# Kernel tuning notes

Measured on AMD Instinct MI355X. Metric: run time of the kernel, lower is better.

The kernel has to match this reference:

```python
import jax, jax.numpy as jnp
import numpy as np

SIZE = 128
WIN = SIZE // 4   # sliding-window size == region size (32)
HALF = WIN // 2   # 16


def _conv(x, w, pad, groups=1):
    return jax.lax.conv_general_dilated(x, w, (1, 1), [(pad, pad), (pad, pad)],
        dimension_numbers=('NCHW', 'OIHW', 'NCHW'), feature_group_count=groups)


def _resize(x, h, w):
    # F.interpolate(..., mode='bilinear', align_corners=False)
    return jax.image.resize(x, (x.shape[0], x.shape[1], h, w), 'bilinear', antialias=False)


def _gauss_kernels():
    ax = np.linspace(-2.0, 2.0, 5)
    xx, yy = np.meshgrid(ax, ax)
    g = np.exp(-(xx ** 2 + yy ** 2) / 2.0) / (2.0 * np.pi)  # sigma = 1
    gx = (-xx * g).astype(np.float32)
    gy = (-yy * g).astype(np.float32)
    return (jnp.asarray(np.tile(gx[None, None], (3, 3, 1, 1))),
            jnp.asarray(np.tile(gy[None, None], (3, 3, 1, 1))))


def _edge_extract(x):
    Gx, Gy = _gauss_kernels()
    h = _conv(x, Gx, 2)
    v = _conv(x, Gy, 2)
    return jnp.tanh(jnp.sqrt(h * h + v * v + 1e-8))


def _color_moments(x, win=5):
    # F.unfold-based local mean / unbiased var / skewness, via depthwise box sums
    C = x.shape[1]
    n = float(win * win)
    ones = jnp.ones((C, 1, win, win), x.dtype)
    box = lambda z: _conv(z, ones, win // 2, groups=C)
    s1 = box(x); s2 = box(x * x); s3 = box(x * x * x)
    mean = s1 / n
    var = (s2 - n * mean * mean) / (n - 1.0)               # unbiased, matches torch.var
    m3 = (s3 - 3.0 * mean * s2 + 2.0 * n * mean ** 3) / n  # E[(x-m)^3]
    skew = m3 / (jnp.sqrt(jnp.maximum(var, 0.0)) ** 3 + 1e-6)
    return jnp.concatenate([mean, var, skew], 1)


def _locate_region(c):
    # scipy: gradient magnitude < 0.2 -> 4-connected label at argmax -> bbox center
    H, W = c.shape
    flat = jnp.argmax(c)
    xm = (flat // W).astype(jnp.int32)
    ym = (flat % W).astype(jnp.int32)
    gm = jnp.hypot(jnp.gradient(c, axis=0), jnp.gradient(c, axis=1))
    mask = gm < 0.2
    seed = jnp.zeros((H, W), bool).at[xm, ym].set(True) & mask

    def dil(r):
        d = r
        d = d | jnp.pad(r[1:, :], ((0, 1), (0, 0)))
        d = d | jnp.pad(r[:-1, :], ((1, 0), (0, 0)))
        d = d | jnp.pad(r[:, 1:], ((0, 0), (0, 1)))
        d = d | jnp.pad(r[:, :-1], ((0, 0), (1, 0)))
        return d & mask

    def body(s):
        r, _ = s
        nr = dil(r)
        return (nr, jnp.any(nr != r))

    region, _ = jax.lax.while_loop(lambda s: s[1], body, (seed, jnp.any(seed)))
    rows = jnp.any(region, 1); cols = jnp.any(region, 0)
    rs = jnp.argmax(rows); re = H - jnp.argmax(rows[::-1])
    cs = jnp.argmax(cols); ce = W - jnp.argmax(cols[::-1])
    ok = mask[xm, ym]  # label_at_max != 0
    x1 = jnp.where(ok, ((rs + re) // 2).astype(jnp.int32), xm)
    y1 = jnp.where(ok, ((cs + ce) // 2).astype(jnp.int32), ym)
    return x1, y1


def _affine_grid(move, H, W):
    # theta = [[1,0,tx],[0,1,ty]] with (tx,ty)=move, align_corners=False
    bx = (2.0 * jnp.arange(W, dtype=jnp.float32) + 1.0) / W - 1.0
    by = (2.0 * jnp.arange(H, dtype=jnp.float32) + 1.0) / H - 1.0
    gx = bx[None, None, :] + move[:, 0, None, None]
    gy = by[None, :, None] + move[:, 1, None, None]
    return jnp.stack(jnp.broadcast_arrays(gx, gy), -1)  # [B,H,W,2]


def _grid_sample(x, grid):
    # bilinear, zeros padding, align_corners=False (torch defaults)
    B, C, H, W = x.shape
    ix = ((grid[..., 0] + 1.0) * W - 1.0) / 2.0
    iy = ((grid[..., 1] + 1.0) * H - 1.0) / 2.0
    ix0 = jnp.floor(ix).astype(jnp.int32)
    iy0 = jnp.floor(iy).astype(jnp.int32)
    wx1 = ix - ix0; wy1 = iy - iy0
    b = jnp.arange(B)[:, None, None]

    def g(yy, xx):
        valid = ((xx >= 0) & (xx < W) & (yy >= 0) & (yy < H)).astype(x.dtype)
        v = x[b, :, jnp.clip(yy, 0, H - 1), jnp.clip(xx, 0, W - 1)]  # [B,Hg,Wg,C]
        return v * valid[..., None]

    out = (g(iy0, ix0) * ((1 - wy1) * (1 - wx1))[..., None]
         + g(iy0, ix0 + 1) * ((1 - wy1) * wx1)[..., None]
         + g(iy0 + 1, ix0) * (wy1 * (1 - wx1))[..., None]
         + g(iy0 + 1, ix0 + 1) * (wy1 * wx1)[..., None])
    return jnp.transpose(out, (0, 3, 1, 2))


def _bn_relu6(x, w, b):
    # BatchNorm2d in training mode (batch stats, biased var, eps=1e-5) + ReLU6
    m = x.mean((0, 2, 3), keepdims=True)
    v = ((x - m) ** 2).mean((0, 2, 3), keepdims=True)
    y = (x - m) / jnp.sqrt(v + 1e-5) * w[None, :, None, None] + b[None, :, None, None]
    return jnp.clip(y, 0.0, 6.0)


def setup_inputs():
    key = jax.random.key(0)
    ks = jax.random.split(key, 8)
    B, C = 8, 64
    return dict(
        warm_flag=1,
        feat1=jax.random.normal(ks[0], (B, C, SIZE, SIZE), jnp.float32),
        feat2=jax.random.normal(ks[1], (B, C, SIZE, SIZE), jnp.float32),
        cam1=jax.random.uniform(ks[2], (B, 64, 64), jnp.float32),
        cam2=jax.random.uniform(ks[3], (B, 64, 64), jnp.float32),
        f_g=jax.random.uniform(ks[4], (B, 3, 512, 512), jnp.float32),
        f_e=jax.random.uniform(ks[5], (B, 3, 512, 512), jnp.float32),
        conv1_w=jax.random.normal(ks[6], (C, 3, 3, 3), jnp.float32) * 0.1,
        conv1_b=jnp.zeros((C,), jnp.float32),
        conv2_w=jax.random.normal(ks[7], (C, 9, 3, 3), jnp.float32) * 0.1,
        conv2_b=jnp.zeros((C,), jnp.float32),
        bn_w=jnp.ones((C,), jnp.float32),
        bn_b=jnp.zeros((C,), jnp.float32),
    )


def reference(warm_flag, feat1, feat2, cam1, cam2, f_g, f_e,
              conv1_w, conv1_b, conv2_w, conv2_b, bn_w, bn_b):
    B = cam1.shape[0]
    c1 = _resize(cam1[:, None], SIZE, SIZE)
    c2 = _resize(cam2[:, None], SIZE, SIZE)

    if warm_flag == 1:
        # numpy/scipy path in torch is detached from autograd
        c1s = jax.lax.stop_gradient(c1)
        c2s = jax.lax.stop_gradient(c2)
        x1, y1 = jax.vmap(_locate_region)(c1s[:, 0])
        # valid-mode box convolution of cam2 with ones((H//4, W//4)), argmax
        box = jax.lax.conv_general_dilated(c2s, jnp.ones((1, 1, WIN, WIN), c2.dtype), (1, 1),
            'VALID', dimension_numbers=('NCHW', 'OIHW', 'NCHW'))[:, 0]
        Wv = box.shape[-1]
        flat = jnp.argmax(box.reshape(B, -1), -1)
        x2 = (flat // Wv + HALF).astype(jnp.int32)
        y2 = (flat % Wv + HALF).astype(jnp.int32)

        idx = jnp.arange(SIZE)
        def rect(xc, yc):
            r = (idx[None, :] >= jnp.maximum(xc - HALF, 0)[:, None]) & \
                (idx[None, :] < jnp.minimum(xc + HALF, SIZE)[:, None])
            cc = (idx[None, :] >= jnp.maximum(yc - HALF, 0)[:, None]) & \
                 (idx[None, :] < jnp.minimum(yc + HALF, SIZE)[:, None])
            return r[:, None, :, None] & cc[:, None, None, :]
        mask1 = rect(x1, y1).astype(feat1.dtype)
        mask2 = rect(x2, y2).astype(feat2.dtype)
        mi1 = jnp.stack([x1, y1], -1).astype(jnp.float32)
        mi2 = jnp.stack([x2, y2], -1).astype(jnp.float32)
    else:
        mask1 = jnp.zeros_like(feat1)
        mask2 = jnp.zeros_like(feat2)
        mi1 = jnp.zeros((B, 2), jnp.float32)
        mi2 = jnp.zeros((B, 2), jnp.float32)

    cam2_move = (mi2 - mi1) / (SIZE // 2)
    cam1_move = (mi1 - mi2) / (SIZE // 2)
    grid1 = _affine_grid(cam1_move, SIZE, SIZE)
    grid2 = _affine_grid(cam2_move, SIZE, SIZE)

    moments = _resize(_color_moments(f_e), SIZE, SIZE)   # [B,9,128,128]
    edge = _resize(_edge_extract(f_g), SIZE, SIZE)       # [B,3,128,128]
    feat1_edge = jnp.clip(_conv(edge, conv1_w, 1) + conv1_b[None, :, None, None], 0.0, 6.0)
    feat2_color = _conv(moments, conv2_w, 1) + conv2_b[None, :, None, None]

    feat2_move = _grid_sample(feat2_color * mask2, grid2)
    feat1_edge_move = _grid_sample(feat1_edge * mask1, grid1)

    Bc, C, H, W = feat1.shape
    f1 = feat1.reshape(Bc, C, -1)
    f2 = feat2.reshape(Bc, C, -1)
    f2m = feat2_move.reshape(Bc, C, -1)
    f1m = feat1_edge_move.reshape(Bc, C, -1)

    f2_attn = jax.nn.softmax(jnp.einsum('bcn,bdn->bcd', f2m, f1), -1)  # [B,C,C]
    feat1_apply = jnp.einsum('bcd,bdn->bcn', f2_attn, f1).reshape(Bc, C, H, W)
    f1_attn = jax.nn.softmax(jnp.einsum('bcn,bdn->bcd', f1m, f2), -1)
    feat2_apply = jnp.einsum('bcd,bdn->bcn', f1_attn, f2).reshape(Bc, C, H, W)

    feat1_apply = _bn_relu6(feat1_apply, bn_w, bn_b)
    feat2_apply = _bn_relu6(feat2_apply, bn_w, bn_b)

    if warm_flag == 0:
        return (feat1, feat2, grid1, grid2, feat1_edge, feat2_color, f1_attn, f2_attn, feat1, feat2)
    return (feat1_apply, feat2_apply, grid1, grid2, feat1_edge, feat2_color, f1_attn, f2_attn, feat1, feat2)
```

## Files before the change

kernel.cpp:

```cpp
#include <hip/hip_runtime.h>
#include <math.h>

#define SIZE 128
#define WIN 32
#define HALF 16
#define B 8
#define C 64
#define N (SIZE*SIZE)
#define BCN 8388608
#define BV 97

#define O_APPLY1   0
#define O_APPLY2   8388608
#define O_GRID1    16777216
#define O_GRID2    17039360
#define O_EDGEF    17301504
#define O_COLORF   25690112
#define O_ATTN1    34078720
#define O_ATTN2    34111488
#define O_FEAT1    34144256
#define O_FEAT2    42532864

#define WS_BNP     0
#define WS_XY      361472
#define WS_MOM     361600
#define WS_EDGE    1541248
#define WS_BN      1737856

#define NEGINF (-3.402823466e+38f)

typedef unsigned __int128 u128;

__device__ __forceinline__ u128 hfill(u128 g, u128 m) {
  u128 p = m;
  g |= p & (g << 1);  p &= p << 1;
  g |= p & (g << 2);  p &= p << 2;
  g |= p & (g << 4);  p &= p << 4;
  g |= p & (g << 8);  p &= p << 8;
  g |= p & (g << 16); p &= p << 16;
  g |= p & (g << 32); p &= p << 32;
  g |= p & (g << 64);
  p = m;
  g |= p & (g >> 1);  p &= p >> 1;
  g |= p & (g >> 2);  p &= p >> 2;
  g |= p & (g >> 4);  p &= p >> 4;
  g |= p & (g >> 8);  p &= p >> 8;
  g |= p & (g >> 16); p &= p >> 16;
  g |= p & (g >> 32); p &= p >> 32;
  g |= p & (g >> 64);
  return g;
}

__global__ __launch_bounds__(256) void k_front(
    const float* __restrict__ cam1, const float* __restrict__ cam2,
    int* __restrict__ xy, float* __restrict__ g1, float* __restrict__ g2) {
  int b = blockIdx.x, tid = threadIdx.x;
  __shared__ float sc[N];
  __shared__ float sc2[N];
  __shared__ float sv[256]; __shared__ int si[256];
  __shared__ unsigned int maskw[512];
  __shared__ unsigned long long glo[128], ghi[128];
  __shared__ unsigned long long rowany[2];
  __shared__ int s_changed, s_xm, s_ym, s_ok;
  __shared__ int s_x1, s_y1, s_x2, s_y2;

  const float* src1 = cam1 + b * 4096;
  const float* src2 = cam2 + b * 4096;

  float bv = NEGINF; int bi = 0;
  for (int k = 0; k < 64; ++k) {
    int pix = k * 256 + tid;
    int i = pix >> 7, j = pix & 127;
    float fy = fminf(fmaxf(0.5f * (float)i - 0.25f, 0.f), 63.f);
    float fx = fminf(fmaxf(0.5f * (float)j - 0.25f, 0.f), 63.f);
    int y0 = (int)fy; float ty = fy - (float)y0; int y1i = min(y0 + 1, 63);
    int x0 = (int)fx; float tx = fx - (float)x0; int x1i = min(x0 + 1, 63);
    float a00 = src1[y0 * 64 + x0],  a01 = src1[y0 * 64 + x1i];
    float a10 = src1[y1i * 64 + x0], a11 = src1[y1i * 64 + x1i];
    float v1 = (1.f - ty) * ((1.f - tx) * a00 + tx * a01)
             + ty * ((1.f - tx) * a10 + tx * a11);
    float c00 = src2[y0 * 64 + x0],  c01 = src2[y0 * 64 + x1i];
    float c10 = src2[y1i * 64 + x0], c11 = src2[y1i * 64 + x1i];
    float v2 = (1.f - ty) * ((1.f - tx) * c00 + tx * c01)
             + ty * ((1.f - tx) * c10 + tx * c11);
    sc[pix] = v1; sc2[pix] = v2;
    if (v1 > bv) { bv = v1; bi = pix; }
  }
  sv[tid] = bv; si[tid] = bi;
  __syncthreads();
  for (int s = 128; s; s >>= 1) {
    if (tid < s) {
      float ov = sv[tid + s]; int oi = si[tid + s];
      if (ov > sv[tid] || (ov == sv[tid] && oi < si[tid])) { sv[tid] = ov; si[tid] = oi; }
    }
    __syncthreads();
  }
  if (tid == 0) { s_xm = si[0] >> 7; s_ym = si[0] & 127; }

  #pragma unroll
  for (int q = 0; q < 2; ++q) {
    int w = tid + q * 256;
    int row = w >> 2, cb = (w & 3) * 32;
    unsigned int m = 0;
    for (int bit = 0; bit < 32; ++bit) {
      int i = row, j = cb + bit;
      float gx_, gy_;
      if (i == 0)        gx_ = sc[128 + j] - sc[j];
      else if (i == 127) gx_ = sc[127 * 128 + j] - sc[126 * 128 + j];
      else               gx_ = 0.5f * (sc[(i + 1) * 128 + j] - sc[(i - 1) * 128 + j]);
      if (j == 0)        gy_ = sc[i * 128 + 1] - sc[i * 128];
      else if (j == 127) gy_ = sc[i * 128 + 127] - sc[i * 128 + 126];
      else               gy_ = 0.5f * (sc[i * 128 + j + 1] - sc[i * 128 + j - 1]);
      if (hypotf(gx_, gy_) < 0.2f) m |= (1u << bit);
    }
    maskw[w] = m;
  }
  __syncthreads();
  if (tid == 0) {
    int w = (s_xm << 2) + (s_ym >> 5), bit = s_ym & 31;
    s_ok = (maskw[w] >> bit) & 1;
  }
  __syncthreads();

  int r = tid;
  u128 m = 0, g = 0;
  if (tid < 128) {
    m = ((u128)maskw[r * 4])
      | ((u128)maskw[r * 4 + 1] << 32)
      | ((u128)maskw[r * 4 + 2] << 64)
      | ((u128)maskw[r * 4 + 3] << 96);
    if (s_ok && r == s_xm) g = ((u128)1) << s_ym;
    g = hfill(g, m);
  }
  for (;;) {
    if (tid == 0) s_changed = 0;
    if (tid < 128) { glo[r] = (unsigned long long)g; ghi[r] = (unsigned long long)(g >> 64); }
    __syncthreads();
    if (tid < 128) {
      u128 gn = g;
      if (r > 0)   gn |= ((u128)glo[r - 1]) | ((u128)ghi[r - 1] << 64);
      if (r < 127) gn |= ((u128)glo[r + 1]) | ((u128)ghi[r + 1] << 64);
      gn &= m;
      gn = hfill(gn, m);
      if (gn != g) { g = gn; s_changed = 1; }
    }
    __syncthreads();
    if (!s_changed) break;
  }

  if (tid < 128) {
    unsigned long long ba = __ballot(g != 0);
    if ((tid & 63) == 0) rowany[tid >> 6] = ba;
    glo[r] = (unsigned long long)g; ghi[r] = (unsigned long long)(g >> 64);
  }
  __syncthreads();
  if (tid == 0) {
    unsigned long long r0 = rowany[0], r1 = rowany[1];
    unsigned long long cl = 0, ch = 0;
    for (int i = 0; i < 128; ++i) { cl |= glo[i]; ch |= ghi[i]; }
    int rs = 0, re = 0, cs = 0, ce = 0;
    if (r0 | r1) {
      rs = r0 ? (__ffsll(r0) - 1) : 64 + (__ffsll(r1) - 1);
      re = r1 ? 128 - __clzll(r1) : 64 - __clzll(r0);
      cs = cl ? (__ffsll(cl) - 1) : 64 + (__ffsll(ch) - 1);
      ce = ch ? 128 - __clzll(ch) : 64 - __clzll(cl);
    }
    int x1, y1;
    if (s_ok) { x1 = (rs + re) >> 1; y1 = (cs + ce) >> 1; }
    else      { x1 = s_xm;           y1 = s_ym; }
    xy[b] = x1; xy[8 + b] = y1; s_x1 = x1; s_y1 = y1;
  }
  __syncthreads();

  for (int idx = tid; idx < BV * 128; idx += 256) {
    int rr = idx >> 7, cc = idx & 127;
    float acc = 0.f;
    #pragma unroll
    for (int dy = 0; dy < WIN; ++dy) acc += sc2[(rr + dy) * 128 + cc];
    sc[idx] = acc;
  }
  __syncthreads();

  bv = NEGINF; bi = 0;
  for (int p = tid; p < BV * BV; p += 256) {
    int rr = p / BV, cc = p % BV;
    float s = 0.f;
    #pragma unroll
    for (int dx = 0; dx < WIN; ++dx) s += sc[rr * 128 + cc + dx];
    if (s > bv) { bv = s; bi = p; }
  }
  sv[tid] = bv; si[tid] = bi;
  __syncthreads();
  for (int s = 128; s; s >>= 1) {
    if (tid < s) {
      float ov = sv[tid + s]; int oi = si[tid + s];
      if (ov > sv[tid] || (ov == sv[tid] && oi < si[tid])) { sv[tid] = ov; si[tid] = oi; }
    }
    __syncthreads();
  }
  if (tid == 0) {
    int x2 = si[0] / BV + HALF, y2 = si[0] % BV + HALF;
    xy[16 + b] = x2; xy[24 + b] = y2; s_x2 = x2; s_y2 = y2;
  }
  __syncthreads();

  float x1f = (float)s_x1, y1f = (float)s_y1;
  float x2f = (float)s_x2, y2f = (float)s_y2;
  float m1x = (x1f - x2f) / 64.f, m1y = (y1f - y2f) / 64.f;
  float* g1b = g1 + (size_t)b * N * 2;
  float* g2b = g2 + (size_t)b * N * 2;
  for (int k = 0; k < 64; ++k) {
    int pix = k * 256 + tid;
    int h = pix >> 7, w = pix & 127;
    float bx = (2.f * (float)w + 1.f) / 128.f - 1.f;
    float by = (2.f * (float)h + 1.f) / 128.f - 1.f;
    g1b[pix * 2]     = bx + m1x; g1b[pix * 2 + 1] = by + m1y;
    g2b[pix * 2]     = bx - m1x; g2b[pix * 2 + 1] = by - m1y;
  }
}

__global__ __launch_bounds__(256) void k_prep(const float* __restrict__ fe,
                                              const float* __restrict__ fg,
                                              float* __restrict__ mom,
                                              float* __restrict__ edge) {
  __shared__ float sx[66 * 66];
  int tid = threadIdx.x;
  if (blockIdx.x < 1536) {
    int blk = blockIdx.x;
    int tile = blk & 63, ch = (blk >> 6) % 3, b = blk / 192;
    int ti0 = (tile >> 3) * 16, tj0 = (tile & 7) * 16;
    const float* src = fe + (size_t)(b * 3 + ch) * 262144;
    int oy0 = 4 * ti0 - 1, ox0 = 4 * tj0 - 1;
    for (int l = tid; l < 66 * 66; l += 256) {
      int r = l / 66, cc = l % 66;
      int gy = oy0 + r, gx = ox0 + cc;
      sx[l] = (gy >= 0 && gy < 512 && gx >= 0 && gx < 512) ? src[gy * 512 + gx] : 0.f;
    }
    __syncthreads();
    int ii = tid >> 4, jj = tid & 15;
    int i = ti0 + ii, j = tj0 + jj;
    float s1a[6], s2a[6], s3a[6], s1b[6], s2b[6], s3b[6];
    #pragma unroll
    for (int t = 0; t < 6; ++t) {
      float a1 = 0, a2 = 0, a3 = 0, b1 = 0, b2 = 0, b3 = 0;
      int lx = 4 * jj + t;
      #pragma unroll
      for (int r = 0; r < 6; ++r) {
        float v = sx[(4 * ii + r) * 66 + lx];
        float v2 = v * v, v3 = v2 * v;
        if (r < 5) { a1 += v; a2 += v2; a3 += v3; }
        if (r > 0) { b1 += v; b2 += v2; b3 += v3; }
      }
      s1a[t] = a1; s2a[t] = a2; s3a[t] = a3;
      s1b[t] = b1; s2b[t] = b2; s3b[t] = b3;
    }
    float am = 0, av = 0, as = 0;
    #pragma unroll
    for (int py = 0; py < 2; ++py) {
      #pragma unroll
      for (int px = 0; px < 2; ++px) {
        float s1 = 0, s2 = 0, s3 = 0;
        #pragma unroll
        for (int t = 0; t < 5; ++t) {
          s1 += py ? s1b[px + t] : s1a[px + t];
          s2 += py ? s2b[px + t] : s2a[px + t];
          s3 += py ? s3b[px + t] : s3a[px + t];
        }
        float mean = s1 / 25.f;
        float var  = (s2 - 25.f * mean * mean) / 24.f;
        float m3   = (s3 - 3.f * mean * s2 + 50.f * mean * mean * mean) / 25.f;
        float sq   = sqrtf(fmaxf(var, 0.f));
        float skew = m3 / (sq * sq * sq + 1e-6f);
        am += mean; av += var; as += skew;
      }
    }
    int base = (b * 9 + ch) * N + i * 128 + j;
    mom[base]         = 0.25f * am;
    mom[base + 3 * N] = 0.25f * av;
    mom[base + 6 * N] = 0.25f * as;
  } else {
    int blk = blockIdx.x - 1536;
    int tile = blk & 63, b = blk >> 6;
    int ti0 = (tile >> 3) * 16, tj0 = (tile & 7) * 16;
    const float* s0 = fg + (size_t)b * 3 * 262144;
    int oy0 = 4 * ti0 - 1, ox0 = 4 * tj0 - 1;
    for (int l = tid; l < 66 * 66; l += 256) {
      int r = l / 66, cc = l % 66;
      int gy = oy0 + r, gx = ox0 + cc;
      float v = 0.f;
      if (gy >= 0 && gy < 512 && gx >= 0 && gx < 512) {
        int o = gy * 512 + gx;
        v = s0[o] + s0[262144 + o] + s0[524288 + o];
      }
      sx[l] = v;
    }
    __syncthreads();
    int ii = tid >> 4, jj = tid & 15;
    int i = ti0 + ii, j = tj0 + jj;
    const float INV2PI = 0.15915494309189535f;
    float wg[5], ug[5];
    #pragma unroll
    for (int t = 0; t < 5; ++t) {
      float a = (float)t - 2.f;
      float e = expf(-0.5f * a * a);
      wg[t] = e; ug[t] = -a * e;
    }
    float rAa[6], rAb[6], rBa[6], rBb[6];
    #pragma unroll
    for (int t = 0; t < 6; ++t) {
      float aa = 0, ab = 0, ba = 0, bb = 0;
      int lx = 4 * jj + t;
      #pragma unroll
      for (int r = 0; r < 6; ++r) {
        float v = sx[(4 * ii + r) * 66 + lx];
        if (r < 5) { aa += v * wg[r]; ba += v * ug[r]; }
        if (r > 0) { ab += v * wg[r - 1]; bb += v * ug[r - 1]; }
      }
      rAa[t] = aa; rAb[t] = ab; rBa[t] = ba; rBb[t] = bb;
    }
    float acc = 0.f;
    #pragma unroll
    for (int py = 0; py < 2; ++py) {
      #pragma unroll
      for (int px = 0; px < 2; ++px) {
        float h = 0, v = 0;
        #pragma unroll
        for (int t = 0; t < 5; ++t) {
          float A  = py ? rAb[px + t] : rAa[px + t];
          float Bw = py ? rBb[px + t] : rBa[px + t];
          h += A * ug[t];
          v += Bw * wg[t];
        }
        h *= INV2PI; v *= INV2PI;
        acc += tanhf(sqrtf(h * h + v * v + 1e-8f));
      }
    }
    edge[b * N + i * 128 + j] = 0.25f * acc;
  }
}

__global__ __launch_bounds__(256) void k_conv12(
    const float* __restrict__ edge, const float* __restrict__ w1,
    const float* __restrict__ b1, float* __restrict__ o4,
    const float* __restrict__ mom, const float* __restrict__ w2,
    const float* __restrict__ b2, float* __restrict__ o5) {
  __shared__ float tin[9 * 324];
  __shared__ float wsm[64 * 84];
  int b = blockIdx.x >> 6, tile = blockIdx.x & 63;
  int ti0 = (tile >> 3) * 16, tj0 = (tile & 7) * 16;
  int tid = threadIdx.x;
  int i = tid >> 4, j = tid & 15;
  if (blockIdx.y == 0) {
    for (int l = tid; l < 324; l += 256) {
      int r = l / 18, cc = l % 18;
      int gi = ti0 + r - 1, gj = tj0 + cc - 1;
      tin[l] = (gi >= 0 && gi < 128 && gj >= 0 && gj < 128) ? edge[b * N + gi * 128 + gj] : 0.f;
    }
    for (int l = tid; l < 64 * 12; l += 256) {
      int o = l / 12, t = l % 12;
      wsm[l] = (t < 9) ? (w1[o * 27 + t] + w1[o * 27 + 9 + t] + w1[o * 27 + 18 + t]) : 0.f;
    }
    __syncthreads();
    float win[12];
    #pragma unroll
    for (int dy = 0; dy < 3; ++dy)
      #pragma unroll
      for (int dx = 0; dx < 3; ++dx)
        win[dy * 3 + dx] = tin[(i + dy) * 18 + (j + dx)];
    win[9] = 0.f; win[10] = 0.f; win[11] = 0.f;
    float* o = o4 + (size_t)b * C * N + (ti0 + i) * 128 + tj0 + j;
    for (int oc = 0; oc < C; ++oc) {
      const float4* wr = (const float4*)(wsm + oc * 12);
      float acc = b1[oc];
      #pragma unroll
      for (int q = 0; q < 3; ++q) {
        float4 w4 = wr[q];
        acc += w4.x * win[4 * q] + w4.y * win[4 * q + 1]
             + w4.z * win[4 * q + 2] + w4.w * win[4 * q + 3];
      }
      o[oc * N] = fminf(fmaxf(acc, 0.f), 6.f);
    }
  } else {
    for (int l = tid; l < 9 * 324; l += 256) {
      int ic = l / 324, rem = l % 324, r = rem / 18, cc = rem % 18;
      int gi = ti0 + r - 1, gj = tj0 + cc - 1;
      tin[l] = (gi >= 0 && gi < 128 && gj >= 0 && gj < 128) ? mom[(b * 9 + ic) * N + gi * 128 + gj] : 0.f;
    }
    for (int l = tid; l < 64 * 84; l += 256) {
      int o = l / 84, t = l % 84;
      wsm[l] = (t < 81) ? w2[o * 81 + t] : 0.f;
    }
    __syncthreads();
    float win[84];
    #pragma unroll
    for (int ic = 0; ic < 9; ++ic)
      #pragma unroll
      for (int dy = 0; dy < 3; ++dy)
        #pragma unroll
        for (int dx = 0; dx < 3; ++dx)
          win[ic * 9 + dy * 3 + dx] = tin[ic * 324 + (i + dy) * 18 + (j + dx)];
    win[81] = 0.f; win[82] = 0.f; win[83] = 0.f;
    float* o = o5 + (size_t)b * C * N + (ti0 + i) * 128 + tj0 + j;
    for (int oc = 0; oc < C; ++oc) {
      const float4* wr = (const float4*)(wsm + oc * 84);
      float acc = b2[oc];
      #pragma unroll
      for (int q = 0; q < 21; ++q) {
        float4 w4 = wr[q];
        acc += w4.x * win[4 * q] + w4.y * win[4 * q + 1]
             + w4.z * win[4 * q + 2] + w4.w * win[4 * q + 3];
      }
      o[oc * N] = acc;
    }
  }
}

__global__ __launch_bounds__(256) void k_logits(const float* __restrict__ aB1,
                                                const float* __restrict__ bB1,
                                                const float* __restrict__ aB2,
                                                const float* __restrict__ bB2,
                                                float* __restrict__ lg,
                                                const int* __restrict__ xy) {
  int mode = blockIdx.y;
  const float* aBase = mode ? aB2 : aB1;
  const float* bBase = mode ? bB2 : bB1;
  int b = blockIdx.x >> 4, sl = blockIdx.x & 15;
  int tid = threadIdx.x;
  int ci = (tid >> 4) << 2, di = (tid & 15) << 2;
  float* o = lg + (size_t)(((mode * 8 + b) * 16 + sl)) * 4096;

  int x1 = xy[b], y1 = xy[8 + b], x2 = xy[16 + b], y2 = xy[24 + b];
  int dyh, dxw, rlo, rhi, clo, chi;
  if (mode == 0) {
    dyh = y1 - y2; dxw = x1 - x2;
    rlo = max(x1 - HALF, 0); rhi = min(x1 + HALF, SIZE);
    clo = max(y1 - HALF, 0); chi = min(y1 + HALF, SIZE);
  } else {
    dyh = y2 - y1; dxw = x2 - x1;
    rlo = max(x2 - HALF, 0); rhi = min(x2 + HALF, SIZE);
    clo = max(y2 - HALF, 0); chi = min(y2 + HALF, SIZE);
  }
  int hlo = max(0, rlo - dyh), hhi = min(SIZE, rhi - dyh);
  int wlo = max(0, clo - dxw), whi = min(SIZE, chi - dxw);
  int wn = whi - wlo, hn = hhi - hlo;
  int npos = (wn > 0 && hn > 0) ? wn * hn : 0;
  if (sl * 64 >= npos) {
    #pragma unroll
    for (int u = 0; u < 4; ++u)
      #pragma unroll
      for (int v = 0; v < 4; ++v)
        o[(ci + u) * 64 + (di + v)] = 0.f;
    return;
  }

  __shared__ float aS[64][65];
  __shared__ float bS[64][65];
  const float* aB = aBase + (size_t)b * C * N;
  const float* bB = bBase + (size_t)b * C * N;
  for (int l = tid; l < 4096; l += 256) {
    int ch = l >> 6, k = l & 63;
    int p = sl * 64 + k;
    float av = 0.f, bv = 0.f;
    if (p < npos) {
      int h = hlo + p / wn, w = wlo + p % wn;
      av = aB[ch * N + (h + dyh) * 128 + (w + dxw)];
      bv = bB[ch * N + h * 128 + w];
    }
    aS[ch][k] = av; bS[ch][k] = bv;
  }
  __syncthreads();
  float acc[4][4] = {};
  #pragma unroll 4
  for (int k = 0; k < 64; ++k) {
    float a0 = aS[ci][k], a1 = aS[ci + 1][k], a2 = aS[ci + 2][k], a3 = aS[ci + 3][k];
    float b0 = bS[di][k], b1v = bS[di + 1][k], b2v = bS[di + 2][k], b3 = bS[di + 3][k];
    acc[0][0] += a0 * b0; acc[0][1] += a0 * b1v; acc[0][2] += a0 * b2v; acc[0][3] += a0 * b3;
    acc[1][0] += a1 * b0; acc[1][1] += a1 * b1v; acc[1][2] += a1 * b2v; acc[1][3] += a1 * b3;
    acc[2][0] += a2 * b0; acc[2][1] += a2 * b1v; acc[2][2] += a2 * b2v; acc[2][3] += a2 * b3;
    acc[3][0] += a3 * b0; acc[3][1] += a3 * b1v; acc[3][2] += a3 * b2v; acc[3][3] += a3 * b3;
  }
  #pragma unroll
  for (int u = 0; u < 4; ++u)
    #pragma unroll
    for (int v = 0; v < 4; ++v)
      o[(ci + u) * 64 + (di + v)] = acc[u][v];
}

__global__ void k_softmax(const float* __restrict__ lg,
                          float* __restrict__ o6, float* __restrict__ o7) {
  int row = blockIdx.x;
  int mode = blockIdx.y;
  float* dst = mode ? o7 : o6;
  int b = row >> 6, c = row & 63;
  int lane = threadIdx.x;
  const float* base = lg + (size_t)((mode * 8 + b) * 16) * 4096 + c * 64 + lane;
  float v = 0.f;
  #pragma unroll
  for (int sl = 0; sl < 16; ++sl) v += base[sl * 4096];
  float mx = v;
  for (int off = 32; off; off >>= 1) mx = fmaxf(mx, __shfl_xor(mx, off));
  float e = expf(v - mx);
  float s = e;
  for (int off = 32; off; off >>= 1) s += __shfl_xor(s, off);
  dst[row * 64 + lane] = e / s;
}

__global__ __launch_bounds__(256) void k_applyst(const float* __restrict__ a1,
                                                 const float* __restrict__ s1_,
                                                 float* __restrict__ d1,
                                                 const float* __restrict__ a2,
                                                 const float* __restrict__ s2_,
                                                 float* __restrict__ d2,
                                                 float* __restrict__ bnp) {
  const float* attn; const float* src; float* dst;
  int t = blockIdx.y;
  if (t == 0) { attn = a1; src = s1_; dst = d1; }
  else        { attn = a2; src = s2_; dst = d2; }
  int b = blockIdx.x >> 6, chunk = blockIdx.x & 63;
  int n0 = chunk * 256 + threadIdx.x;
  const float* s = src + (size_t)b * C * N + n0;
  float v[64];
  #pragma unroll
  for (int d = 0; d < 64; ++d) v[d] = s[d * N];
  const float4* at4 = (const float4*)(attn + b * 4096);
  float* o = dst + (size_t)b * C * N + n0;
  __shared__ float red[64][4], red2[64][4];
  int lane = threadIdx.x & 63, wave = threadIdx.x >> 6;
  for (int c = 0; c < 64; ++c) {
    float acc = 0.f;
    #pragma unroll
    for (int q = 0; q < 16; ++q) {
      float4 w4 = at4[c * 16 + q];
      acc += w4.x * v[4 * q] + w4.y * v[4 * q + 1] + w4.z * v[4 * q + 2] + w4.w * v[4 * q + 3];
    }
    o[c * N] = acc;
    float sr = acc, ssr = acc * acc;
    for (int off = 32; off; off >>= 1) {
      sr  += __shfl_xor(sr, off);
      ssr += __shfl_xor(ssr, off);
    }
    if (lane == 0) { red[c][wave] = sr; red2[c][wave] = ssr; }
  }
  __syncthreads();
  if (threadIdx.x < 64) {
    int c = threadIdx.x;
    float sr  = red[c][0] + red[c][1] + red[c][2] + red[c][3];
    float ssr = red2[c][0] + red2[c][1] + red2[c][2] + red2[c][3];
    int idx = (t * 64 + c) * 512 + blockIdx.x;
    bnp[idx]         = sr;
    bnp[65536 + idx] = ssr;
  }
}

__global__ void k_bnstats2(const float* __restrict__ bnp, float* __restrict__ stats) {
  __shared__ float sr[128][4], ssr[128][4];
  int tid = threadIdx.x;
  int combo = tid >> 2, q = tid & 3;
  float s = 0.f, ss = 0.f;
  for (int k = 0; k < 128; ++k) {
    int idx = combo * 512 + q * 128 + k;
    s  += bnp[idx];
    ss += bnp[65536 + idx];
  }
  sr[combo][q] = s; ssr[combo][q] = ss;
  __syncthreads();
  if (q == 0) {
    float S  = sr[combo][0] + sr[combo][1] + sr[combo][2] + sr[combo][3];
    float SS = ssr[combo][0] + ssr[combo][1] + ssr[combo][2] + ssr[combo][3];
    int t = combo >> 6, c = combo & 63;
    float mean = S / 131072.f;
    float var  = SS / 131072.f - mean * mean;
    stats[t * 128 + c]      = mean;
    stats[t * 128 + 64 + c] = 1.f / sqrtf(var + 1e-5f);
  }
}

__global__ __launch_bounds__(256) void k_final(
    const float4* __restrict__ f1, float4* __restrict__ o8,
    const float4* __restrict__ f2, float4* __restrict__ o9,
    float4* __restrict__ o0, float4* __restrict__ o1,
    const float* __restrict__ stats,
    const float* __restrict__ bw, const float* __restrict__ bb) {
  int i = blockIdx.x * 256 + threadIdx.x;
  int t = blockIdx.y;
  if (t == 0) o8[i] = f1[i]; else o9[i] = f2[i];
  float4* p = t ? o1 : o0;
  int c = (i >> 12) & 63;
  float m = stats[t * 128 + c], r = stats[t * 128 + 64 + c];
  float w_ = bw[c], b_ = bb[c];
  float4 v = p[i];
  v.x = fminf(fmaxf((v.x - m) * r * w_ + b_, 0.f), 6.f);
  v.y = fminf(fmaxf((v.y - m) * r * w_ + b_, 0.f), 6.f);
  v.z = fminf(fmaxf((v.z - m) * r * w_ + b_, 0.f), 6.f);
  v.w = fminf(fmaxf((v.w - m) * r * w_ + b_, 0.f), 6.f);
  p[i] = v;
}

extern "C" void kernel_launch(void* const* d_in, const int* in_sizes, int n_in,
                              void* d_out, int out_size, void* d_ws, size_t ws_size,
                              hipStream_t stream) {
  const float* feat1   = (const float*)d_in[1];
  const float* feat2   = (const float*)d_in[2];
  const float* cam1    = (const float*)d_in[3];
  const float* cam2    = (const float*)d_in[4];
  const float* f_g     = (const float*)d_in[5];
  const float* f_e     = (const float*)d_in[6];
  const float* conv1_w = (const float*)d_in[7];
  const float* conv1_b = (const float*)d_in[8];
  const float* conv2_w = (const float*)d_in[9];
  const float* conv2_b = (const float*)d_in[10];
  const float* bn_w    = (const float*)d_in[11];
  const float* bn_b    = (const float*)d_in[12];

  float* out = (float*)d_out;
  float* w = (float*)d_ws;
  int* xy = (int*)(w + WS_XY);

  float* o0 = out + O_APPLY1;
  float* o1 = out + O_APPLY2;
  float* o2 = out + O_GRID1;
  float* o3 = out + O_GRID2;
  float* o4 = out + O_EDGEF;
  float* o5 = out + O_COLORF;
  float* o6 = out + O_ATTN1;
  float* o7 = out + O_ATTN2;
  float* o8 = out + O_FEAT1;
  float* o9 = out + O_FEAT2;

  k_front<<<B, 256, 0, stream>>>(cam1, cam2, xy, o2, o3);

  k_prep<<<2048, 256, 0, stream>>>(f_e, f_g, w + WS_MOM, w + WS_EDGE);

  k_conv12<<<dim3(B * 64, 2), 256, 0, stream>>>(w + WS_EDGE, conv1_w, conv1_b, o4,
                                                w + WS_MOM, conv2_w, conv2_b, o5);

  k_logits<<<dim3(B * 16, 2), 256, 0, stream>>>(o4, feat2, o5, feat1,
                                                w + WS_MOM, xy);

  k_softmax<<<dim3(B * C, 2), 64, 0, stream>>>(w + WS_MOM, o6, o7);

  k_applyst<<<dim3(B * 64, 2), 256, 0, stream>>>(o7, feat1, o0, o6, feat2, o1,
                                                 w + WS_BNP);

  k_bnstats2<<<1, 512, 0, stream>>>(w + WS_BNP, w + WS_BN);

  k_final<<<dim3(BCN / 4 / 256, 2), 256, 0, stream>>>(
      (const float4*)feat1, (float4*)o8, (const float4*)feat2, (float4*)o9,
      (float4*)o0, (float4*)o1, w + WS_BN, bn_w, bn_b);
}
```

Before: 635.6 us.

## Build gradient mask via wave ballots and run flood fill within one wavefront

The threshold mask is now computed one pixel per thread and packed with wavefront ballots into 64-bit words, replacing the per-thread 32-bit serial loop. The 4-connected flood fill runs entirely inside a single 64-lane wavefront, with each lane owning two rows. Rows exchange state through shuffles and the loop exits via __any, so the block-wide __syncthreads inside the iteration loop is gone. The bounding-box reduction also uses shuffles instead of a serial loop on thread 0. In exchange, other waves sit idle while the fill runs, and each lane does more serial hfill work per iteration.

```diff
diff --git a/kernel.cpp b/kernel.cpp
--- a/kernel.cpp
+++ b/kernel.cpp
@@ -58,10 +58,8 @@
   __shared__ float sc[N];
   __shared__ float sc2[N];
   __shared__ float sv[256]; __shared__ int si[256];
-  __shared__ unsigned int maskw[512];
-  __shared__ unsigned long long glo[128], ghi[128];
-  __shared__ unsigned long long rowany[2];
-  __shared__ int s_changed, s_xm, s_ym, s_ok;
+  __shared__ unsigned long long mask64[256];
+  __shared__ int s_xm, s_ym, s_ok;
   __shared__ int s_x1, s_y1, s_x2, s_y2;
 
   const float* src1 = cam1 + b * 4096;
@@ -96,79 +94,78 @@
     __syncthreads();
   }
   if (tid == 0) { s_xm = si[0] >> 7; s_ym = si[0] & 127; }
-
-  #pragma unroll
-  for (int q = 0; q < 2; ++q) {
-    int w = tid + q * 256;
-    int row = w >> 2, cb = (w & 3) * 32;
-    unsigned int m = 0;
-    for (int bit = 0; bit < 32; ++bit) {
-      int i = row, j = cb + bit;
-      float gx_, gy_;
-      if (i == 0)        gx_ = sc[128 + j] - sc[j];
-      else if (i == 127) gx_ = sc[127 * 128 + j] - sc[126 * 128 + j];
-      else               gx_ = 0.5f * (sc[(i + 1) * 128 + j] - sc[(i - 1) * 128 + j]);
-      if (j == 0)        gy_ = sc[i * 128 + 1] - sc[i * 128];
-      else if (j == 127) gy_ = sc[i * 128 + 127] - sc[i * 128 + 126];
-      else               gy_ = 0.5f * (sc[i * 128 + j + 1] - sc[i * 128 + j - 1]);
-      if (hypotf(gx_, gy_) < 0.2f) m |= (1u << bit);
-    }
-    maskw[w] = m;
+  __syncthreads();
+
+  for (int k = 0; k < 64; ++k) {
+    int pix = k * 256 + tid;
+    int i = pix >> 7, j = pix & 127;
+    float gx_, gy_;
+    if (i == 0)        gx_ = sc[128 + j] - sc[j];
+    else if (i == 127) gx_ = sc[127 * 128 + j] - sc[126 * 128 + j];
+    else               gx_ = 0.5f * (sc[(i + 1) * 128 + j] - sc[(i - 1) * 128 + j]);
+    if (j == 0)        gy_ = sc[i * 128 + 1] - sc[i * 128];
+    else if (j == 127) gy_ = sc[i * 128 + 127] - sc[i * 128 + 126];
+    else               gy_ = 0.5f * (sc[i * 128 + j + 1] - sc[i * 128 + j - 1]);
+    bool pred = hypotf(gx_, gy_) < 0.2f;
+    unsigned long long bal = __ballot(pred);
+    if ((tid & 63) == 0) mask64[(i << 1) + (j >> 6)] = bal;
   }
   __syncthreads();
   if (tid == 0) {
-    int w = (s_xm << 2) + (s_ym >> 5), bit = s_ym & 31;
-    s_ok = (maskw[w] >> bit) & 1;
-  }
-  __syncthreads();
-
-  int r = tid;
-  u128 m = 0, g = 0;
-  if (tid < 128) {
-    m = ((u128)maskw[r * 4])
-      | ((u128)maskw[r * 4 + 1] << 32)
-      | ((u128)maskw[r * 4 + 2] << 64)
-      | ((u128)maskw[r * 4 + 3] << 96);
-    if (s_ok && r == s_xm) g = ((u128)1) << s_ym;
-    g = hfill(g, m);
-  }
-  for (;;) {
-    if (tid == 0) s_changed = 0;
-    if (tid < 128) { glo[r] = (unsigned long long)g; ghi[r] = (unsigned long long)(g >> 64); }
-    __syncthreads();
-    if (tid < 128) {
-      u128 gn = g;
-      if (r > 0)   gn |= ((u128)glo[r - 1]) | ((u128)ghi[r - 1] << 64);
-      if (r < 127) gn |= ((u128)glo[r + 1]) | ((u128)ghi[r + 1] << 64);
-      gn &= m;
-      gn = hfill(gn, m);
-      if (gn != g) { g = gn; s_changed = 1; }
-    }
-    __syncthreads();
-    if (!s_changed) break;
-  }
-
-  if (tid < 128) {
-    unsigned long long ba = __ballot(g != 0);
-    if ((tid & 63) == 0) rowany[tid >> 6] = ba;
-    glo[r] = (unsigned long long)g; ghi[r] = (unsigned long long)(g >> 64);
-  }
-  __syncthreads();
-  if (tid == 0) {
-    unsigned long long r0 = rowany[0], r1 = rowany[1];
-    unsigned long long cl = 0, ch = 0;
-    for (int i = 0; i < 128; ++i) { cl |= glo[i]; ch |= ghi[i]; }
-    int rs = 0, re = 0, cs = 0, ce = 0;
-    if (r0 | r1) {
-      rs = r0 ? (__ffsll(r0) - 1) : 64 + (__ffsll(r1) - 1);
-      re = r1 ? 128 - __clzll(r1) : 64 - __clzll(r0);
-      cs = cl ? (__ffsll(cl) - 1) : 64 + (__ffsll(ch) - 1);
-      ce = ch ? 128 - __clzll(ch) : 64 - __clzll(cl);
-    }
-    int x1, y1;
-    if (s_ok) { x1 = (rs + re) >> 1; y1 = (cs + ce) >> 1; }
-    else      { x1 = s_xm;           y1 = s_ym; }
-    xy[b] = x1; xy[8 + b] = y1; s_x1 = x1; s_y1 = y1;
+    unsigned long long wdd = mask64[(s_xm << 1) + (s_ym >> 6)];
+    s_ok = (int)((wdd >> (s_ym & 63)) & 1ull);
+  }
+  __syncthreads();
+
+  if (tid < 64) {
+    int l = tid;
+    u128 m0 = ((u128)mask64[4 * l])     | ((u128)mask64[4 * l + 1] << 64);
+    u128 m1 = ((u128)mask64[4 * l + 2]) | ((u128)mask64[4 * l + 3] << 64);
+    u128 g0 = 0, g1v = 0;
+    if (s_ok && (s_xm >> 1) == l) {
+      if ((s_xm & 1) == 0) g0  = ((u128)1) << s_ym;
+      else                 g1v = ((u128)1) << s_ym;
+    }
+    g0  = hfill(g0 & m0, m0);
+    g1v = hfill(g1v & m1, m1);
+    for (;;) {
+      unsigned long long ulo = __shfl_up((unsigned long long)g1v, 1);
+      unsigned long long uhi = __shfl_up((unsigned long long)(g1v >> 64), 1);
+      u128 up = (l > 0) ? (((u128)ulo) | ((u128)uhi << 64)) : (u128)0;
+      unsigned long long dlo = __shfl_down((unsigned long long)g0, 1);
+      unsigned long long dhi = __shfl_down((unsigned long long)(g0 >> 64), 1);
+      u128 dn = (l < 63) ? (((u128)dlo) | ((u128)dhi << 64)) : (u128)0;
+      u128 n0 = hfill((g0 | up | g1v) & m0, m0);
+      u128 n1 = hfill((g1v | n0 | dn) & m1, m1);
+      bool chg = (n0 != g0) || (n1 != g1v);
+      g0 = n0; g1v = n1;
+      if (!__any(chg)) break;
+    }
+    unsigned long long be = __ballot(g0 != 0);
+    unsigned long long bo = __ballot(g1v != 0);
+    unsigned long long cl = (unsigned long long)(g0 | g1v);
+    unsigned long long chh = (unsigned long long)((g0 | g1v) >> 64);
+    for (int off = 32; off; off >>= 1) {
+      cl  |= __shfl_xor(cl, off);
+      chh |= __shfl_xor(chh, off);
+    }
+    if (l == 0) {
+      int rs = 0, re = 0, cs = 0, ce = 0;
+      if (be | bo) {
+        int af = be ? (__ffsll(be) - 1) : 1000;
+        int bf = bo ? (__ffsll(bo) - 1) : 1000;
+        rs = min(af * 2, bf * 2 + 1);
+        int al = be ? (63 - __clzll(be)) : -1000;
+        int bl = bo ? (63 - __clzll(bo)) : -1000;
+        re = max(al * 2, bl * 2 + 1) + 1;
+        cs = cl ? (__ffsll(cl) - 1) : 64 + (__ffsll(chh) - 1);
+        ce = chh ? 128 - __clzll(chh) : 64 - __clzll(cl);
+      }
+      int x1, y1;
+      if (s_ok) { x1 = (rs + re) >> 1; y1 = (cs + ce) >> 1; }
+      else      { x1 = s_xm;           y1 = s_ym; }
+      xy[b] = x1; xy[8 + b] = y1; s_x1 = x1; s_y1 = y1;
+    }
   }
   __syncthreads();
 
```

After: 631.5 us. No clear change (-0.6%).
